# Kernel tuning notes

Measured on AMD Instinct MI355X. Metric: run time of the kernel, lower is better.

## Reference

```python
import jax, jax.numpy as jnp
import numpy as np

EPS = 1e-3  # matches eps=0.001 in __init__


def p2o(psf, H, W):
    """PSF -> OTF: zero-pad to (H,W), roll so kernel center is at origin, FFT2."""
    B, C, kh, kw = psf.shape
    otf = jnp.zeros((B, C, H, W), psf.dtype).at[:, :, :kh, :kw].set(psf)
    otf = jnp.roll(otf, (-(kh // 2), -(kw // 2)), axis=(-2, -1))
    return jnp.fft.fft2(otf)


def splits_mean(a, sf):
    """Mean over the sf*sf distinct blocks of splits(): contiguous-chunk split
    via view(sf, H/sf, sf, W/sf); mean over the two sf axes equals mean over
    the scale^2 trailing dim of the original splits output."""
    B, C, H, W = a.shape
    return a.reshape(B, C, sf, H // sf, sf, W // sf).mean(axis=(2, 4))


def setup_inputs() -> dict:
    key = jax.random.key(0)
    kx, kk = jax.random.split(key)
    x = jax.random.normal(kx, (4, 64, 128, 128), dtype=jnp.float32)
    k = jax.random.uniform(kk, (4, 64, 25, 25), dtype=jnp.float32)
    alpha = jnp.zeros((1, 64, 1, 1), dtype=jnp.float32)  # learned parameter
    return {"x": x, "k": k, "alpha": alpha, "sf": 2}


def reference(x, k, alpha, sf):
    biaseps = jax.nn.sigmoid(alpha - 9.0) + EPS          # (1,C,1,1)
    B, C, h, w = x.shape
    H, W = h * sf, w * sf
    # s-fold zero-fill upsample (STy)
    STy = jnp.zeros((B, C, H, W), x.dtype).at[:, :, ::sf, ::sf].set(x)
    # nearest-neighbor interpolate by sf
    xu = jnp.repeat(jnp.repeat(x, sf, axis=-2), sf, axis=-1) if sf != 1 else x
    FB = p2o(k, H, W)                                    # complex (B,C,H,W)
    FBC = jnp.conj(FB)
    F2B = jnp.abs(FB) ** 2
    FBFy = FBC * jnp.fft.fft2(STy)
    FR = FBFy + jnp.fft.fft2(biaseps * xu)
    FBR = splits_mean(FB * FR, sf)                       # (B,C,H/sf,W/sf)
    invW = splits_mean(F2B, sf)
    invWBR = FBR / (invW + biaseps)
    FCBinvWBR = FBC * jnp.tile(invWBR, (1, 1, sf, sf))   # repeat(1,1,sf,sf)
    FX = (FR - FCBinvWBR) / biaseps
    return jnp.real(jnp.fft.ifft2(FX))
```

## Files before the change

kernel.cpp:

```cpp
#include <hip/hip_runtime.h>
#include <math.h>


static __device__ __forceinline__ float2 cmul(float2 a, float2 b) {
    return make_float2(a.x * b.x - a.y * b.y, a.x * b.y + a.y * b.x);
}
static __device__ __forceinline__ float2 cadd(float2 a, float2 b) {
    return make_float2(a.x + b.x, a.y + b.y);
}
static __device__ __forceinline__ float2 conjf2(float2 a) {
    return make_float2(a.x, -a.y);
}

template <int HB, int SIGN, int THREADS>
static __device__ __forceinline__ void fill_tw(float2* tw) {
    for (int i = threadIdx.x; i < HB; i += THREADS) {
        float s, c;
        __sincosf((float)SIGN * (float)M_PI * (float)i / (float)HB, &s, &c);
        tw[i] = make_float2(c, s);
    }
}

template <int N, int R, int SIGN>
static __device__ __forceinline__ int fft_lds_rows(float2 (&buf)[2][R][N],
                                                   const float2* __restrict__ tw) {
    constexpr int HB = N / 2;
    const int tid = threadIdx.x;
    const int row = tid / HB;
    const int bt = tid % HB;
    int cur = 0, m = 1;
    for (int l = HB; l >= 1; l >>= 1) {
        __syncthreads();
        const int k = bt & (m - 1);
        const float2 w = tw[bt - k];
        float2 a = buf[cur][row][bt];
        float2 b = buf[cur][row][bt + HB];
        float2 d = make_float2(a.x - b.x, a.y - b.y);
        float2 wd = make_float2(w.x * d.x - w.y * d.y, w.x * d.y + w.y * d.x);
        const int o = 2 * bt - k;
        buf[cur ^ 1][row][o] = make_float2(a.x + b.x, a.y + b.y);
        buf[cur ^ 1][row][o + m] = wd;
        cur ^= 1;
        m <<= 1;
    }
    __syncthreads();
    return cur;
}

template <int N, int TC, int SIGN, int THREADS>
static __device__ __forceinline__ int fft_lds_cols(float2 (&buf)[2][N][TC],
                                                   const float2* __restrict__ tw) {
    constexpr int HB = N / 2;
    constexpr int WORK = HB * TC;
    const int tid = threadIdx.x;
    int cur = 0, m = 1;
    for (int l = HB; l >= 1; l >>= 1) {
        __syncthreads();
        for (int w0 = tid; w0 < WORK; w0 += THREADS) {
            const int col = w0 % TC;
            const int bt = w0 / TC;
            const int k = bt & (m - 1);
            const float2 w = tw[bt - k];
            float2 a = buf[cur][bt][col];
            float2 b = buf[cur][bt + HB][col];
            float2 d = make_float2(a.x - b.x, a.y - b.y);
            float2 wd = make_float2(w.x * d.x - w.y * d.y, w.x * d.y + w.y * d.x);
            const int o = 2 * bt - k;
            buf[cur ^ 1][o][col] = make_float2(a.x + b.x, a.y + b.y);
            buf[cur ^ 1][o + m][col] = wd;
        }
        cur ^= 1;
        m <<= 1;
    }
    __syncthreads();
    return cur;
}

__global__ __launch_bounds__(256) void k1_fft_rows_x(const float* __restrict__ x,
                                                     float2* __restrict__ Fx) {
    __shared__ float2 buf[2][4][128];
    __shared__ float2 tw64m[64];
    const int tid = threadIdx.x;
    const int row = tid >> 6;
    const int t = tid & 63;
    fill_tw<64, -1, 256>(tw64m);
    const int gpair = blockIdx.x * 4 + row;
    const float* r0 = x + (size_t)gpair * 256;
    const float* r1 = r0 + 128;
    const float2 a0 = ((const float2*)r0)[t];
    const float2 a1 = ((const float2*)r1)[t];
    buf[0][row][2 * t].x = a0.x;
    buf[0][row][2 * t].y = a1.x;
    buf[0][row][2 * t + 1].x = a0.y;
    buf[0][row][2 * t + 1].y = a1.y;
    int cur = fft_lds_rows<128, 4, -1>(buf, tw64m);
    float2* d0 = Fx + (size_t)gpair * 256;
    float2* d1 = d0 + 128;
    for (int h = 0; h < 2; ++h) {
        int tt = t + h * 64;
        float2 Zt = buf[cur][row][tt];
        float2 Zm = buf[cur][row][(128 - tt) & 127];
        d0[tt] = make_float2(0.5f * (Zt.x + Zm.x), 0.5f * (Zt.y - Zm.y));
        float ax = Zt.x - Zm.x, ay = Zt.y + Zm.y;
        d1[tt] = make_float2(0.5f * ay, -0.5f * ax);
    }
}

__global__ __launch_bounds__(256) void k2_fft_cols_x(float2* __restrict__ Fx) {
    __shared__ float2 buf[2][128][16];
    __shared__ float2 tw64m[64];
    const int tid = threadIdx.x;
    const int img = blockIdx.x >> 3;
    const int c0 = (blockIdx.x & 7) * 16;
    fill_tw<64, -1, 256>(tw64m);
    float2* base = Fx + (size_t)img * 16384 + c0;
    for (int it = 0; it < 8; ++it) {
        int idx = it * 256 + tid;
        buf[0][idx >> 4][idx & 15] = base[(idx >> 4) * 128 + (idx & 15)];
    }
    int cur = fft_lds_cols<128, 16, -1, 256>(buf, tw64m);
    for (int it = 0; it < 8; ++it) {
        int idx = it * 256 + tid;
        base[(idx >> 4) * 128 + (idx & 15)] = buf[cur][idx >> 4][idx & 15];
    }
}

__global__ __launch_bounds__(128) void k3_fft_rows_k(const float* __restrict__ kin,
                                                     float2* __restrict__ FBtmp) {
    __shared__ float2 buf[2][1][256];
    __shared__ float2 tw128m[128];
    const int tid = threadIdx.x;
    const int img = blockIdx.x / 25;
    const int lr = blockIdx.x % 25;
    fill_tw<128, -1, 128>(tw128m);
    const float* krow = kin + img * 625 + lr * 25;
    for (int h = 0; h < 2; ++h) {
        int v = tid + h * 128;
        int pc = (v + 12) & 255;
        buf[0][0][v] = make_float2(pc < 25 ? krow[pc] : 0.f, 0.f);
    }
    int cur = fft_lds_rows<256, 1, -1>(buf, tw128m);
    float2* dst = FBtmp + (size_t)img * 6400 + lr * 256;
    dst[tid] = buf[cur][0][tid];
    dst[tid + 128] = buf[cur][0][tid + 128];
}

__global__ __launch_bounds__(256) void k4_dft_cols_k(const float2* __restrict__ FBtmp,
                                                     float2* __restrict__ FBh) {
    __shared__ float2 T[33][28];
    const int j = threadIdx.x;
    const int img = blockIdx.x >> 2;
    const int q = blockIdx.x & 3;
    const int ubeg = q * 33;
    const int nu = (ubeg + 33 < 129) ? 33 : (129 - ubeg);
    const float k2pi = -2.f * (float)M_PI / 256.f;

    for (int idx = j; idx < nu * 25; idx += 256) {
        const int ul = idx / 25;
        const int p = idx - ul * 25;
        const int u = ubeg + ul;
        float s, c;
        __sincosf(k2pi * (float)((u * (p + 244)) & 255), &s, &c);
        T[ul][p] = make_float2(c, s);
    }

    const float2* src = FBtmp + (size_t)img * 6400 + j;
    float2 S[25];
#pragma unroll
    for (int p = 0; p < 25; ++p) S[p] = src[p * 256];
    __syncthreads();

    float2* dst = FBh + (size_t)img * 33024 + j;
    for (int ul = 0; ul < nu; ++ul) {
        float2 a0 = make_float2(0.f, 0.f);
        float2 a1 = make_float2(0.f, 0.f);
#pragma unroll
        for (int p = 0; p < 25; ++p) {
            const float2 t = T[ul][p];
            const float2 s = S[p];
            if (p & 1) {
                a1.x = fmaf(t.x, s.x, fmaf(-t.y, s.y, a1.x));
                a1.y = fmaf(t.x, s.y, fmaf(t.y, s.x, a1.y));
            } else {
                a0.x = fmaf(t.x, s.x, fmaf(-t.y, s.y, a0.x));
                a0.y = fmaf(t.x, s.y, fmaf(t.y, s.x, a0.y));
            }
        }
        dst[(size_t)(ubeg + ul) * 256] = make_float2(a0.x + a1.x, a0.y + a1.y);
    }
}

__global__ __launch_bounds__(256) void k6_fused(const float2* __restrict__ FBh,
                                                const float2* __restrict__ Fx,
                                                const float* __restrict__ alpha,
                                                float2* __restrict__ Zf) {
    __shared__ float2 stage[2][256];
    __shared__ float2 buf[2][2][256];
    __shared__ float2 twp[128];
    const int tid = threadIdx.x;
    const int row = tid >> 7;
    const int t = tid & 127;
    const int img = blockIdx.x / 65;
    const int p = blockIdx.x % 65;
    fill_tw<128, 1, 256>(twp);
    const int r = p, rp = 128 - p;
    const float2* base = FBh + (size_t)img * 33024;
    stage[0][tid] = base[r * 256 + tid];
    stage[1][tid] = base[rp * 256 + tid];
    __syncthreads();

    const int u = (row == 0) ? p : (128 - p);
    const int um = u & 127;
    const int mi = (um == p) ? 0 : 1;
    const int oi = 1 - mi;

    float2 f00 = stage[mi][t];
    float2 f01 = stage[mi][t + 128];
    float2 f10, f11;
    if (um == 0) {
        f10 = stage[oi][t];
        f11 = stage[oi][t + 128];
    } else {
        f10 = conjf2(stage[oi][(256 - t) & 255]);
        f11 = conjf2(stage[oi][128 - t]);
    }
    float2 fx = Fx[(size_t)img * 16384 + um * 128 + t];

    const float ci = twp[um].x, si = -twp[um].y;
    const float cj = twp[t].x, sj = -twp[t].y;
    float2 Di0 = make_float2(1.f + ci, si);
    float2 Di1 = make_float2(1.f - ci, -si);
    float2 Dj0 = make_float2(1.f + cj, sj);
    float2 Dj1 = make_float2(1.f - cj, -sj);
    float2 S1 = cadd(cadd(cmul(cmul(f00, Di0), Dj0), cmul(cmul(f10, Di1), Dj0)),
                     cadd(cmul(cmul(f01, Di0), Dj1), cmul(cmul(f11, Di1), Dj1)));
    S1.x *= 0.25f;
    S1.y *= 0.25f;
    float S2 = 0.25f * (f00.x * f00.x + f00.y * f00.y + f01.x * f01.x + f01.y * f01.y +
                        f10.x * f10.x + f10.y * f10.y + f11.x * f11.x + f11.y * f11.y);
    float b = 1.f / (1.f + __expf(9.f - alpha[img & 63])) + 1e-3f;
    float inv = 1.f / (S2 + b);
    float2 mm = make_float2((1.f - S1.x) * inv, (-S1.y) * inv);

    float2 c0v = (u < 128) ? f00 : f10;
    float2 c1v = (u < 128) ? f01 : f11;
    float2 Du = (u < 128) ? make_float2(1.f + ci, si) : make_float2(1.f - ci, -si);
    float2 Dv0 = make_float2(1.f + cj, sj);
    float2 Dv1 = make_float2(1.f - cj, -sj);
    const float scale = 1.f / 65536.f;
    float2 t0 = cadd(cmul(conjf2(c0v), mm), cmul(Du, Dv0));
    float2 t1 = cadd(cmul(conjf2(c1v), mm), cmul(Du, Dv1));
    float2 FX0 = cmul(fx, t0);
    float2 FX1 = cmul(fx, t1);
    buf[0][row][t] = make_float2(FX0.x * scale, FX0.y * scale);
    buf[0][row][t + 128] = make_float2(FX1.x * scale, FX1.y * scale);
    int cur = fft_lds_rows<256, 2, 1>(buf, twp);

    const int u0 = u;
    const bool dowrite = (row == 0) || (p > 0 && p < 64);
    if (dowrite) {
        const float2 w = twp[u0];
        float2* zb = Zf + (size_t)img * 32768 + (size_t)u0 * 256;
        for (int h = 0; h < 2; ++h) {
            int jj = t + h * 128;
            float2 su = buf[cur][row][jj];
            float2 s2 = buf[cur][row ^ 1][jj];
            float2 e = make_float2(su.x + s2.x, su.y - s2.y);
            float2 o = make_float2(su.x - s2.x, su.y + s2.y);
            float2 wo = make_float2(w.x * o.x - w.y * o.y, w.x * o.y + w.y * o.x);
            zb[jj] = make_float2(e.x - wo.y, e.y + wo.x);
        }
    }
}

__global__ __launch_bounds__(256) void k7_c2r(const float2* __restrict__ Zf,
                                              float* __restrict__ out) {
    __shared__ float2 buf[2][128][16];
    __shared__ float2 tw64p[64];
    const int tid = threadIdx.x;
    const int img = blockIdx.x >> 4;
    const int c0 = (blockIdx.x & 15) * 16;
    fill_tw<64, 1, 256>(tw64p);
    const float2* zb = Zf + (size_t)img * 32768 + c0;
    for (int it = 0; it < 8; ++it) {
        int idx = it * 256 + tid;
        buf[0][idx >> 4][idx & 15] = zb[(idx >> 4) * 256 + (idx & 15)];
    }
    int cur = fft_lds_cols<128, 16, 1, 256>(buf, tw64p);
    float* ob = out + (size_t)img * 65536 + c0;
    for (int it = 0; it < 8; ++it) {
        int idx = it * 256 + tid;
        int n = idx >> 4, c = idx & 15;
        float2 y = buf[cur][n][c];
        ob[(2 * n) * 256 + c] = y.x;
        ob[(2 * n + 1) * 256 + c] = y.y;
    }
}

extern "C" void kernel_launch(void* const* d_in, const int* in_sizes, int n_in,
                              void* d_out, int out_size, void* d_ws, size_t ws_size,
                              hipStream_t stream) {
    const float* x = (const float*)d_in[0];
    const float* k = (const float*)d_in[1];
    const float* alpha = (const float*)d_in[2];
    float* out = (float*)d_out;

    float2* Fx = (float2*)d_ws;
    float2* FBh = Fx + 256 * 16384;
    float2* Zf = FBh + 256 * 33024;
    float2* FBtmp = Zf + 256 * 32768;

    hipLaunchKernelGGL(k1_fft_rows_x, dim3(4096), dim3(256), 0, stream, x, Fx);
    hipLaunchKernelGGL(k2_fft_cols_x, dim3(2048), dim3(256), 0, stream, Fx);
    hipLaunchKernelGGL(k3_fft_rows_k, dim3(6400), dim3(128), 0, stream, k, FBtmp);
    hipLaunchKernelGGL(k4_dft_cols_k, dim3(1024), dim3(256), 0, stream, FBtmp, FBh);
    hipLaunchKernelGGL(k6_fused, dim3(256 * 65), dim3(256), 0, stream, FBh, Fx, alpha, Zf);
    hipLaunchKernelGGL(k7_c2r, dim3(4096), dim3(256), 0, stream, Zf, out);
}
```

Before: 204.5 us.

## Use radix-4 FFT stages in column and fused row kernels, pairing rows per block

Replaces the radix-2 Stockham column FFTs in k2 and k7 with three radix-4 stages plus a final radix-2 stage, which cuts the number of barrier-separated LDS passes. The fused k6 kernel now handles two row pairs per block with 64 threads per 256-point row. It runs four radix-4 stages with a padded LDS index to avoid bank conflicts, and halves the grid size. The trade-off is larger twiddle tables, more LDS per block, and a duplicated row in the last block that has its writes masked off.

Measured after the change: 194.2 us. -5.0%, faster.

```diff
diff --git a/kernel.cpp b/kernel.cpp
--- a/kernel.cpp
+++ b/kernel.cpp
@@ -8,9 +8,13 @@
 static __device__ __forceinline__ float2 cadd(float2 a, float2 b) {
     return make_float2(a.x + b.x, a.y + b.y);
 }
+static __device__ __forceinline__ float2 csub(float2 a, float2 b) {
+    return make_float2(a.x - b.x, a.y - b.y);
+}
 static __device__ __forceinline__ float2 conjf2(float2 a) {
     return make_float2(a.x, -a.y);
 }
+static __device__ __forceinline__ int PHI(int i) { return i + (i >> 3); }
 
 template <int HB, int SIGN, int THREADS>
 static __device__ __forceinline__ void fill_tw(float2* tw) {
@@ -47,31 +51,52 @@
     return cur;
 }
 
-template <int N, int TC, int SIGN, int THREADS>
-static __device__ __forceinline__ int fft_lds_cols(float2 (&buf)[2][N][TC],
-                                                   const float2* __restrict__ tw) {
-    constexpr int HB = N / 2;
-    constexpr int WORK = HB * TC;
+template <int SIGN, int THREADS>
+static __device__ __forceinline__ int fft4_cols_128(float2 (&buf)[2][128][16],
+                                                    const float2* __restrict__ tw) {
     const int tid = threadIdx.x;
     int cur = 0, m = 1;
-    for (int l = HB; l >= 1; l >>= 1) {
+#pragma unroll
+    for (int st = 0; st < 3; ++st) {
         __syncthreads();
-        for (int w0 = tid; w0 < WORK; w0 += THREADS) {
-            const int col = w0 % TC;
-            const int bt = w0 / TC;
-            const int k = bt & (m - 1);
-            const float2 w = tw[bt - k];
-            float2 a = buf[cur][bt][col];
-            float2 b = buf[cur][bt + HB][col];
-            float2 d = make_float2(a.x - b.x, a.y - b.y);
-            float2 wd = make_float2(w.x * d.x - w.y * d.y, w.x * d.y + w.y * d.x);
-            const int o = 2 * bt - k;
-            buf[cur ^ 1][o][col] = make_float2(a.x + b.x, a.y + b.y);
-            buf[cur ^ 1][o + m][col] = wd;
+        for (int w0 = tid; w0 < 512; w0 += THREADS) {
+            const int col = w0 & 15;
+            const int bq = w0 >> 4;
+            const int k = bq & (m - 1);
+            const int jm = bq - k;
+            const float2 w1 = tw[jm];
+            const float2 w2 = tw[2 * jm];
+            const float2 w3 = tw[3 * jm];
+            float2 a0 = buf[cur][bq][col];
+            float2 a1 = buf[cur][bq + 32][col];
+            float2 a2 = buf[cur][bq + 64][col];
+            float2 a3 = buf[cur][bq + 96][col];
+            float2 s02 = cadd(a0, a2), d02 = csub(a0, a2);
+            float2 s13 = cadd(a1, a3), d13 = csub(a1, a3);
+            float2 b0 = cadd(s02, s13), b2 = csub(s02, s13);
+            float2 b1 = make_float2(d02.x - (float)SIGN * d13.y,
+                                    d02.y + (float)SIGN * d13.x);
+            float2 b3 = make_float2(d02.x + (float)SIGN * d13.y,
+                                    d02.y - (float)SIGN * d13.x);
+            const int o = 4 * jm + k;
+            buf[cur ^ 1][o][col] = b0;
+            buf[cur ^ 1][o + m][col] = cmul(w1, b1);
+            buf[cur ^ 1][o + 2 * m][col] = cmul(w2, b2);
+            buf[cur ^ 1][o + 3 * m][col] = cmul(w3, b3);
         }
         cur ^= 1;
-        m <<= 1;
-    }
+        m <<= 2;
+    }
+    __syncthreads();
+    for (int w0 = tid; w0 < 1024; w0 += THREADS) {
+        const int col = w0 & 15;
+        const int bt = w0 >> 4;
+        float2 a = buf[cur][bt][col];
+        float2 b = buf[cur][bt + 64][col];
+        buf[cur ^ 1][bt][col] = cadd(a, b);
+        buf[cur ^ 1][bt + 64][col] = csub(a, b);
+    }
+    cur ^= 1;
     __syncthreads();
     return cur;
 }
@@ -108,17 +133,21 @@
 
 __global__ __launch_bounds__(256) void k2_fft_cols_x(float2* __restrict__ Fx) {
     __shared__ float2 buf[2][128][16];
-    __shared__ float2 tw64m[64];
+    __shared__ float2 tw[96];
     const int tid = threadIdx.x;
     const int img = blockIdx.x >> 3;
     const int c0 = (blockIdx.x & 7) * 16;
-    fill_tw<64, -1, 256>(tw64m);
+    for (int i = tid; i < 96; i += 256) {
+        float s, c;
+        __sincosf(-(float)M_PI * (float)i / 64.f, &s, &c);
+        tw[i] = make_float2(c, s);
+    }
     float2* base = Fx + (size_t)img * 16384 + c0;
     for (int it = 0; it < 8; ++it) {
         int idx = it * 256 + tid;
         buf[0][idx >> 4][idx & 15] = base[(idx >> 4) * 128 + (idx & 15)];
     }
-    int cur = fft_lds_cols<128, 16, -1, 256>(buf, tw64m);
+    int cur = fft4_cols_128<-1, 256>(buf, tw);
     for (int it = 0; it < 8; ++it) {
         int idx = it * 256 + tid;
         base[(idx >> 4) * 128 + (idx & 15)] = buf[cur][idx >> 4][idx & 15];
@@ -194,80 +223,121 @@
                                                 const float2* __restrict__ Fx,
                                                 const float* __restrict__ alpha,
                                                 float2* __restrict__ Zf) {
-    __shared__ float2 stage[2][256];
-    __shared__ float2 buf[2][2][256];
-    __shared__ float2 twp[128];
-    const int tid = threadIdx.x;
-    const int row = tid >> 7;
-    const int t = tid & 127;
-    const int img = blockIdx.x / 65;
-    const int p = blockIdx.x % 65;
-    fill_tw<128, 1, 256>(twp);
-    const int r = p, rp = 128 - p;
-    const float2* base = FBh + (size_t)img * 33024;
-    stage[0][tid] = base[r * 256 + tid];
-    stage[1][tid] = base[rp * 256 + tid];
-    __syncthreads();
-
-    const int u = (row == 0) ? p : (128 - p);
+    __shared__ float2 stage[4][256];
+    __shared__ float2 buf[2][4][288];
+    __shared__ float2 tw[192];
+    const int tid = threadIdx.x;
+    const int rs = tid >> 6;
+    const int q = tid & 63;
+    const int img = blockIdx.x / 33;
+    const int bq = blockIdx.x % 33;
+    const int pa = 2 * bq;
+    const int pb = (pa + 1 < 65) ? (pa + 1) : 64;
+    for (int i = tid; i < 192; i += 256) {
+        float s, c;
+        __sincosf((float)M_PI * (float)i / 128.f, &s, &c);
+        tw[i] = make_float2(c, s);
+    }
+    {
+        const float2* base = FBh + (size_t)img * 33024;
+        stage[0][tid] = base[pa * 256 + tid];
+        stage[1][tid] = base[(128 - pa) * 256 + tid];
+        stage[2][tid] = base[pb * 256 + tid];
+        stage[3][tid] = base[(128 - pb) * 256 + tid];
+    }
+    __syncthreads();
+
+    const int p = (rs < 2) ? pa : pb;
+    const int sb = rs & 2;
+    const int u = ((rs & 1) == 0) ? p : (128 - p);
     const int um = u & 127;
-    const int mi = (um == p) ? 0 : 1;
-    const int oi = 1 - mi;
-
-    float2 f00 = stage[mi][t];
-    float2 f01 = stage[mi][t + 128];
-    float2 f10, f11;
-    if (um == 0) {
-        f10 = stage[oi][t];
-        f11 = stage[oi][t + 128];
-    } else {
-        f10 = conjf2(stage[oi][(256 - t) & 255]);
-        f11 = conjf2(stage[oi][128 - t]);
-    }
-    float2 fx = Fx[(size_t)img * 16384 + um * 128 + t];
-
-    const float ci = twp[um].x, si = -twp[um].y;
-    const float cj = twp[t].x, sj = -twp[t].y;
-    float2 Di0 = make_float2(1.f + ci, si);
-    float2 Di1 = make_float2(1.f - ci, -si);
-    float2 Dj0 = make_float2(1.f + cj, sj);
-    float2 Dj1 = make_float2(1.f - cj, -sj);
-    float2 S1 = cadd(cadd(cmul(cmul(f00, Di0), Dj0), cmul(cmul(f10, Di1), Dj0)),
-                     cadd(cmul(cmul(f01, Di0), Dj1), cmul(cmul(f11, Di1), Dj1)));
-    S1.x *= 0.25f;
-    S1.y *= 0.25f;
-    float S2 = 0.25f * (f00.x * f00.x + f00.y * f00.y + f01.x * f01.x + f01.y * f01.y +
-                        f10.x * f10.x + f10.y * f10.y + f11.x * f11.x + f11.y * f11.y);
-    float b = 1.f / (1.f + __expf(9.f - alpha[img & 63])) + 1e-3f;
-    float inv = 1.f / (S2 + b);
-    float2 mm = make_float2((1.f - S1.x) * inv, (-S1.y) * inv);
-
-    float2 c0v = (u < 128) ? f00 : f10;
-    float2 c1v = (u < 128) ? f01 : f11;
-    float2 Du = (u < 128) ? make_float2(1.f + ci, si) : make_float2(1.f - ci, -si);
-    float2 Dv0 = make_float2(1.f + cj, sj);
-    float2 Dv1 = make_float2(1.f - cj, -sj);
+    const int msel = (um == p) ? 0 : 1;
+    const int mi = sb | msel;
+    const int oi = sb | (1 - msel);
+
+    const float ci = tw[um].x, si = -tw[um].y;
+    const float b = 1.f / (1.f + __expf(9.f - alpha[img & 63])) + 1e-3f;
     const float scale = 1.f / 65536.f;
-    float2 t0 = cadd(cmul(conjf2(c0v), mm), cmul(Du, Dv0));
-    float2 t1 = cadd(cmul(conjf2(c1v), mm), cmul(Du, Dv1));
-    float2 FX0 = cmul(fx, t0);
-    float2 FX1 = cmul(fx, t1);
-    buf[0][row][t] = make_float2(FX0.x * scale, FX0.y * scale);
-    buf[0][row][t + 128] = make_float2(FX1.x * scale, FX1.y * scale);
-    int cur = fft_lds_rows<256, 2, 1>(buf, twp);
+    const float2 Di0 = make_float2(1.f + ci, si);
+    const float2 Di1 = make_float2(1.f - ci, -si);
+    const float2 Du = (u < 128) ? Di0 : Di1;
+#pragma unroll
+    for (int h = 0; h < 2; ++h) {
+        const int t = q + 64 * h;
+        float2 f00 = stage[mi][t];
+        float2 f01 = stage[mi][t + 128];
+        float2 f10, f11;
+        if (um == 0) {
+            f10 = stage[oi][t];
+            f11 = stage[oi][t + 128];
+        } else {
+            f10 = conjf2(stage[oi][(256 - t) & 255]);
+            f11 = conjf2(stage[oi][128 - t]);
+        }
+        float2 fx = Fx[(size_t)img * 16384 + um * 128 + t];
+        const float cj = tw[t].x, sj = -tw[t].y;
+        float2 Dj0 = make_float2(1.f + cj, sj);
+        float2 Dj1 = make_float2(1.f - cj, -sj);
+        float2 A = cadd(cmul(f00, Dj0), cmul(f01, Dj1));
+        float2 Bt = cadd(cmul(f10, Dj0), cmul(f11, Dj1));
+        float2 S1 = cadd(cmul(A, Di0), cmul(Bt, Di1));
+        S1.x *= 0.25f;
+        S1.y *= 0.25f;
+        float S2 = 0.25f * (f00.x * f00.x + f00.y * f00.y + f01.x * f01.x + f01.y * f01.y +
+                            f10.x * f10.x + f10.y * f10.y + f11.x * f11.x + f11.y * f11.y);
+        float inv = 1.f / (S2 + b);
+        float2 mm = make_float2((1.f - S1.x) * inv, (-S1.y) * inv);
+        float2 c0v = (u < 128) ? f00 : f10;
+        float2 c1v = (u < 128) ? f01 : f11;
+        float2 t0 = cadd(cmul(conjf2(c0v), mm), cmul(Du, Dj0));
+        float2 t1 = cadd(cmul(conjf2(c1v), mm), cmul(Du, Dj1));
+        float2 FX0 = cmul(fx, t0);
+        float2 FX1 = cmul(fx, t1);
+        buf[0][rs][PHI(t)] = make_float2(FX0.x * scale, FX0.y * scale);
+        buf[0][rs][PHI(t + 128)] = make_float2(FX1.x * scale, FX1.y * scale);
+    }
+
+    int cur = 0, m = 1;
+#pragma unroll
+    for (int st = 0; st < 4; ++st) {
+        const int k = q & (m - 1);
+        const int jm = q - k;
+        const float2 w1 = tw[jm];
+        const float2 w2 = tw[2 * jm];
+        const float2 w3 = tw[3 * jm];
+        float2 a0 = buf[cur][rs][PHI(q)];
+        float2 a1 = buf[cur][rs][PHI(q + 64)];
+        float2 a2 = buf[cur][rs][PHI(q + 128)];
+        float2 a3 = buf[cur][rs][PHI(q + 192)];
+        float2 s02 = cadd(a0, a2), d02 = csub(a0, a2);
+        float2 s13 = cadd(a1, a3), d13 = csub(a1, a3);
+        float2 b0 = cadd(s02, s13), b2v = csub(s02, s13);
+        float2 b1 = make_float2(d02.x - d13.y, d02.y + d13.x);
+        float2 b3 = make_float2(d02.x + d13.y, d02.y - d13.x);
+        const int o = 4 * jm + k;
+        buf[cur ^ 1][rs][PHI(o)] = b0;
+        buf[cur ^ 1][rs][PHI(o + m)] = cmul(w1, b1);
+        buf[cur ^ 1][rs][PHI(o + 2 * m)] = cmul(w2, b2v);
+        buf[cur ^ 1][rs][PHI(o + 3 * m)] = cmul(w3, b3);
+        cur ^= 1;
+        m <<= 2;
+    }
+    __syncthreads();
 
     const int u0 = u;
-    const bool dowrite = (row == 0) || (p > 0 && p < 64);
+    bool dowrite = ((rs & 1) == 0) ? true : (p > 0 && p < 64);
+    if (pb == pa && rs >= 2) dowrite = false;
     if (dowrite) {
-        const float2 w = twp[u0];
+        const float2 w = tw[u0];
         float2* zb = Zf + (size_t)img * 32768 + (size_t)u0 * 256;
-        for (int h = 0; h < 2; ++h) {
-            int jj = t + h * 128;
-            float2 su = buf[cur][row][jj];
-            float2 s2 = buf[cur][row ^ 1][jj];
+#pragma unroll
+        for (int hh = 0; hh < 4; ++hh) {
+            const int jj = q + 64 * hh;
+            float2 su = buf[cur][rs][PHI(jj)];
+            float2 s2 = buf[cur][rs ^ 1][PHI(jj)];
             float2 e = make_float2(su.x + s2.x, su.y - s2.y);
-            float2 o = make_float2(su.x - s2.x, su.y + s2.y);
-            float2 wo = make_float2(w.x * o.x - w.y * o.y, w.x * o.y + w.y * o.x);
+            float2 o_ = make_float2(su.x - s2.x, su.y + s2.y);
+            float2 wo = cmul(w, o_);
             zb[jj] = make_float2(e.x - wo.y, e.y + wo.x);
         }
     }
@@ -276,17 +346,21 @@
 __global__ __launch_bounds__(256) void k7_c2r(const float2* __restrict__ Zf,
                                               float* __restrict__ out) {
     __shared__ float2 buf[2][128][16];
-    __shared__ float2 tw64p[64];
+    __shared__ float2 tw[96];
     const int tid = threadIdx.x;
     const int img = blockIdx.x >> 4;
     const int c0 = (blockIdx.x & 15) * 16;
-    fill_tw<64, 1, 256>(tw64p);
+    for (int i = tid; i < 96; i += 256) {
+        float s, c;
+        __sincosf((float)M_PI * (float)i / 64.f, &s, &c);
+        tw[i] = make_float2(c, s);
+    }
     const float2* zb = Zf + (size_t)img * 32768 + c0;
     for (int it = 0; it < 8; ++it) {
         int idx = it * 256 + tid;
         buf[0][idx >> 4][idx & 15] = zb[(idx >> 4) * 256 + (idx & 15)];
     }
-    int cur = fft_lds_cols<128, 16, 1, 256>(buf, tw64p);
+    int cur = fft4_cols_128<1, 256>(buf, tw);
     float* ob = out + (size_t)img * 65536 + c0;
     for (int it = 0; it < 8; ++it) {
         int idx = it * 256 + tid;
@@ -314,6 +388,6 @@
     hipLaunchKernelGGL(k2_fft_cols_x, dim3(2048), dim3(256), 0, stream, Fx);
     hipLaunchKernelGGL(k3_fft_rows_k, dim3(6400), dim3(128), 0, stream, k, FBtmp);
     hipLaunchKernelGGL(k4_dft_cols_k, dim3(1024), dim3(256), 0, stream, FBtmp, FBh);
-    hipLaunchKernelGGL(k6_fused, dim3(256 * 65), dim3(256), 0, stream, FBh, Fx, alpha, Zf);
+    hipLaunchKernelGGL(k6_fused, dim3(256 * 33), dim3(256), 0, stream, FBh, Fx, alpha, Zf);
     hipLaunchKernelGGL(k7_c2r, dim3(4096), dim3(256), 0, stream, Zf, out);
 }
```
